# Kernel tuning notes

Hardware: AMD Instinct MI355X
Metric: run time of the kernel (lower is better)

The kernel has to match this reference:

```python
import jax, jax.numpy as jnp
import numpy as np
from jax import lax

D_IN = 512      # input_size
H = 256         # hidden_size
GRU_IN = H + D_IN  # flowdelta_step prepends residual (H) to the input


def setup_inputs() -> dict:
    key = jax.random.key(0)
    kx, k1, k2, k3, k4 = jax.random.split(key, 5)
    B, T = 128, 1024
    x = jax.random.normal(kx, (B, T, D_IN), dtype=jnp.float32)
    # PyTorch GRU parameter layout: weight_ih (3H, in), weight_hh (3H, H),
    # gate order [r, z, n], init U(-1/sqrt(H), 1/sqrt(H))
    s = 1.0 / np.sqrt(H)
    w_ih = jax.random.uniform(k1, (3 * H, GRU_IN), jnp.float32, -s, s)
    w_hh = jax.random.uniform(k2, (3 * H, H), jnp.float32, -s, s)
    b_ih = jax.random.uniform(k3, (3 * H,), jnp.float32, -s, s)
    b_hh = jax.random.uniform(k4, (3 * H,), jnp.float32, -s, s)
    return {"x": x, "w_ih": w_ih, "w_hh": w_hh, "b_ih": b_ih, "b_hh": b_hh}


def reference(x, w_ih, w_hh, b_ih, b_hh):
    # x: (B, T, D). FlowRNN transposes to (T, B, D) and loops over T,
    # feeding one step at a time with carried hidden -> equivalent to a
    # single unidirectional GRU scan whose step input is [residual, x_t],
    # residual_t = h_{t-1} - h_{t-2} (zeros before t=1), logged pre-update.
    B = x.shape[0]
    xs = jnp.swapaxes(x, 0, 1)  # (T, B, D)

    def step(carry, x_t):
        h_prev, res = carry                                  # (B,H), (B,H)
        inp = jnp.concatenate([res, x_t], axis=-1)           # (B, H+D)
        gx = inp @ w_ih.T + b_ih                             # (B, 3H)
        gh = h_prev @ w_hh.T + b_hh                          # (B, 3H)
        r = jax.nn.sigmoid(gx[:, :H] + gh[:, :H])
        z = jax.nn.sigmoid(gx[:, H:2 * H] + gh[:, H:2 * H])
        n = jnp.tanh(gx[:, 2 * H:] + r * gh[:, 2 * H:])
        h_new = (1.0 - z) * n + z * h_prev
        new_res = h_new - h_prev                             # flowdelta
        return (h_new, new_res), (h_new, res)

    h0 = jnp.zeros((B, H), x.dtype)
    res0 = jnp.zeros((B, H), x.dtype)
    _, (outs, ress) = lax.scan(step, (h0, res0), xs)
    output = jnp.swapaxes(outs, 0, 1)           # (B, T, H)
    residual_output = jnp.swapaxes(ress, 0, 1)  # (B, T, H)
    return output, residual_output
```

## Files before the change

kernel.cpp:

```cpp
#include <hip/hip_runtime.h>


typedef __attribute__((ext_vector_type(8))) short bf16x8_t;
typedef __attribute__((ext_vector_type(4))) float f32x4_t;

#define MFMA16(a, b, c) __builtin_amdgcn_mfma_f32_16x16x32_bf16((a), (b), (c), 0, 0, 0)

constexpr int Bb = 128, Tt = 1024, Dd = 512, Hh = 256;
constexpr int Gg = 8;
constexpr int Ss = 8;
constexpr int ROWS = Bb / Gg;
constexpr int Wj = Hh / Ss;

__device__ __forceinline__ short f2bf(float f) {
  union { float f; unsigned int u; } v; v.f = f;
  unsigned int r = v.u + 0x7fffu + ((v.u >> 16) & 1u);
  return (short)(r >> 16);
}

__device__ __forceinline__ bf16x8_t load8_bf(const float* p) {
  const f32x4_t a = *(const f32x4_t*)p;
  const f32x4_t b = *(const f32x4_t*)(p + 4);
  bf16x8_t r;
  r[0] = f2bf(a[0]); r[1] = f2bf(a[1]); r[2] = f2bf(a[2]); r[3] = f2bf(a[3]);
  r[4] = f2bf(b[0]); r[5] = f2bf(b[1]); r[6] = f2bf(b[2]); r[7] = f2bf(b[3]);
  return r;
}

__global__ __launch_bounds__(256, 1)
void flowrnn_scan(const float* __restrict__ x, const float* __restrict__ w_ih,
                  const float* __restrict__ w_hh, const float* __restrict__ b_ih,
                  const float* __restrict__ b_hh, float* __restrict__ out,
                  unsigned int* __restrict__ ws) {
  __shared__ short xstage[ROWS][520];
  __shared__ float accS[ROWS][260];
  __shared__ float hpown[ROWS][Wj];
  __shared__ float biasR[Wj], biasZ[Wj], biasNX[Wj], biasNH[Wj];

  const int tid  = threadIdx.x;
  const int wid  = tid >> 6;
  const int lane = tid & 63;
  const int n16  = lane & 15;
  const int q    = lane >> 4;
  const int g    = blockIdx.x >> 3;
  const int s    = blockIdx.x & 7;
  const int j0   = Wj * s;

  unsigned int* arrive = ws;
  unsigned short* hring = (unsigned short*)(ws + Gg * Tt);
  unsigned short* rring = hring + 2 * Bb * Hh;

  if (tid < Wj) {
    int j = tid;
    biasR[j]  = b_ih[j0 + j]        + b_hh[j0 + j];
    biasZ[j]  = b_ih[256 + j0 + j]  + b_hh[256 + j0 + j];
    biasNX[j] = b_ih[512 + j0 + j];
    biasNH[j] = b_hh[512 + j0 + j];
  }
  ((float*)hpown)[tid] = 0.f;
  ((float*)hpown)[tid + 256] = 0.f;

  bf16x8_t brz[16], bn[8], bxp[16], bxs[8];
  {
    int grow = (wid < 2) ? (j0 + wid * 16 + n16) : (256 + j0 + (wid - 2) * 16 + n16);
    for (int c = 0; c < 8; ++c)
      brz[c] = load8_bf(w_ih + (size_t)grow * 768 + c * 32 + q * 8);
    for (int c = 0; c < 8; ++c)
      brz[8 + c] = load8_bf(w_hh + (size_t)grow * 256 + c * 32 + q * 8);
  }
  if (wid < 2) {
    int grow = 512 + j0 + wid * 16 + n16;
    for (int c = 0; c < 8; ++c)
      bn[c] = load8_bf(w_ih + (size_t)grow * 768 + c * 32 + q * 8);
  } else {
    int grow = 512 + j0 + (wid - 2) * 16 + n16;
    for (int c = 0; c < 8; ++c)
      bn[c] = load8_bf(w_hh + (size_t)grow * 256 + c * 32 + q * 8);
  }
  {
    int tp = (wid == 3) ? 5 : wid * 2;
    int grow = (tp >> 1) * 256 + j0 + (tp & 1) * 16 + n16;
    for (int c = 0; c < 16; ++c)
      bxp[c] = load8_bf(w_ih + (size_t)grow * 768 + 256 + c * 32 + q * 8);
    int ts = (wid < 2) ? 1 : 3;
    int gs = (ts >> 1) * 256 + j0 + (ts & 1) * 16 + n16;
    int cbase = (wid & 1) ? 8 : 0;
    for (int c = 0; c < 8; ++c)
      bxs[c] = load8_bf(w_ih + (size_t)gs * 768 + 256 + (cbase + c) * 32 + q * 8);
  }
  __syncthreads();

  long spin_budget = 30000000;

  for (int t = 0; t < Tt; ++t) {
    {
      int row = tid >> 4, seg = tid & 15;
      const float* xp = x + ((size_t)(g * ROWS + row) * Tt + t) * Dd + seg * 32;
      bf16x8_t v0 = load8_bf(xp);
      bf16x8_t v1 = load8_bf(xp + 8);
      bf16x8_t v2 = load8_bf(xp + 16);
      bf16x8_t v3 = load8_bf(xp + 24);
      bf16x8_t* dst = (bf16x8_t*)&xstage[row][seg * 32];
      dst[0] = v0; dst[1] = v1; dst[2] = v2; dst[3] = v3;
    }
    __syncthreads();

    f32x4_t accP = {0.f, 0.f, 0.f, 0.f}, accSx = {0.f, 0.f, 0.f, 0.f};
    {
      bf16x8_t xa[16];
      for (int c = 0; c < 16; ++c)
        xa[c] = *(const bf16x8_t*)&xstage[n16][c * 32 + q * 8];
      for (int c = 0; c < 16; ++c)
        accP = MFMA16(xa[c], bxp[c], accP);
      int cbase = (wid & 1) ? 8 : 0;
      for (int c = 0; c < 8; ++c)
        accSx = MFMA16(xa[cbase + c], bxs[c], accSx);
    }

    f32x4_t accRZ = {0.f, 0.f, 0.f, 0.f}, accN = {0.f, 0.f, 0.f, 0.f};
    if (t > 0) {
      if (tid == 0) {
        unsigned int* fp = arrive + g * Tt + (t - 1);
        while (__hip_atomic_load(fp, __ATOMIC_RELAXED, __HIP_MEMORY_SCOPE_AGENT) < (unsigned)Ss) {
          __builtin_amdgcn_s_sleep(1);
          if (--spin_budget < 0) break;
        }
        __threadfence();
      }
      __syncthreads();
      const int slot = (t - 1) & 1;
      const unsigned short* hb = hring + (size_t)slot * (Bb * Hh);
      const unsigned short* rb = rring + (size_t)slot * (Bb * Hh);
      const int b = g * ROWS + n16;
      bf16x8_t rf[8], hf[8];
      for (int c = 0; c < 8; ++c) {
        rf[c] = *(const bf16x8_t*)(rb + (size_t)b * Hh + c * 32 + q * 8);
        hf[c] = *(const bf16x8_t*)(hb + (size_t)b * Hh + c * 32 + q * 8);
      }
      for (int c = 0; c < 8; ++c) accRZ = MFMA16(rf[c], brz[c], accRZ);
      for (int c = 0; c < 8; ++c) accRZ = MFMA16(hf[c], brz[8 + c], accRZ);
      if (wid < 2) { for (int c = 0; c < 8; ++c) accN = MFMA16(rf[c], bn[c], accN); }
      else         { for (int c = 0; c < 8; ++c) accN = MFMA16(hf[c], bn[c], accN); }
    }

    {
      const int r0 = q * 4;
      for (int i = 0; i < 4; ++i) accS[r0 + i][wid * 16 + n16] = accRZ[i];
      const int nb = (wid < 2) ? (64 + wid * 16) : (96 + (wid - 2) * 16);
      for (int i = 0; i < 4; ++i) accS[r0 + i][nb + n16] = accN[i];
      const int pc = (wid == 0) ? 128 : (wid == 1) ? 176 : (wid == 2) ? 224 : 240;
      for (int i = 0; i < 4; ++i) accS[r0 + i][pc + n16] = accP[i];
      const int sc = 144 + 16 * wid + ((wid >= 2) ? 16 : 0);
      for (int i = 0; i < 4; ++i) accS[r0 + i][sc + n16] = accSx[i];
    }
    __syncthreads();

    {
      const int row = tid >> 4;
      const int jp = (tid & 15) * 2;
      float hnew[2], resv[2];
      for (int u = 0; u < 2; ++u) {
        const int j = jp + u;
        float ar  = accS[row][j];
        float az  = accS[row][32 + j];
        float anx = accS[row][64 + j];
        float anh = accS[row][96 + j];
        float xr = (j < 16) ? accS[row][128 + j] : (accS[row][144 + j - 16] + accS[row][160 + j - 16]);
        float xz = (j < 16) ? accS[row][176 + j] : (accS[row][192 + j - 16] + accS[row][208 + j - 16]);
        float xn = (j < 16) ? accS[row][224 + j] : accS[row][240 + j - 16];
        float rg = 1.f / (1.f + __expf(-(ar + xr + biasR[j])));
        float zg = 1.f / (1.f + __expf(-(az + xz + biasZ[j])));
        float narg = (anx + xn + biasNX[j]) + rg * (anh + biasNH[j]);
        float e2 = __expf(2.f * narg);
        float ng = 1.f - 2.f / (e2 + 1.f);
        float hp = hpown[row][j];
        float h  = (1.f - zg) * ng + zg * hp;
        hnew[u] = h; resv[u] = h - hp;
        hpown[row][j] = h;
      }
      const int b = g * ROWS + row;
      float* op = out + ((size_t)b * Tt + t) * Hh + j0 + jp;
      op[0] = hnew[0]; op[1] = hnew[1];
      const int slot = t & 1;
      unsigned int hp32 = ((unsigned int)(unsigned short)f2bf(hnew[0])) |
                          ((unsigned int)(unsigned short)f2bf(hnew[1]) << 16);
      unsigned int rp32 = ((unsigned int)(unsigned short)f2bf(resv[0])) |
                          ((unsigned int)(unsigned short)f2bf(resv[1]) << 16);
      unsigned int* hd = (unsigned int*)(hring + (size_t)slot * (Bb * Hh) + (size_t)b * Hh + j0 + jp);
      unsigned int* rd = (unsigned int*)(rring + (size_t)slot * (Bb * Hh) + (size_t)b * Hh + j0 + jp);
      __hip_atomic_store(hd, hp32, __ATOMIC_RELAXED, __HIP_MEMORY_SCOPE_AGENT);
      __hip_atomic_store(rd, rp32, __ATOMIC_RELAXED, __HIP_MEMORY_SCOPE_AGENT);
    }
    __syncthreads();
    if (tid == 0) {
      __threadfence();
      __hip_atomic_fetch_add(arrive + g * Tt + t, 1u, __ATOMIC_RELEASE, __HIP_MEMORY_SCOPE_AGENT);
    }
  }
}

__global__ void flowrnn_resid(const float* __restrict__ out, float* __restrict__ res) {
  size_t i = (size_t)blockIdx.x * blockDim.x + threadIdx.x;
  const size_t total = (size_t)Bb * Tt * (Hh / 4);
  if (i >= total) return;
  const int j4 = (int)(i & 63);
  const int t  = (int)((i >> 6) & 1023);
  const size_t b = i >> 16;
  const f32x4_t* o = (const f32x4_t*)out;
  const size_t base = b * (size_t)Tt * 64 + j4;
  f32x4_t v = {0.f, 0.f, 0.f, 0.f};
  if (t == 1) v = o[base];
  else if (t >= 2) {
    f32x4_t a = o[base + (size_t)(t - 1) * 64];
    f32x4_t c = o[base + (size_t)(t - 2) * 64];
    v = a - c;
  }
  ((f32x4_t*)res)[base + (size_t)t * 64] = v;
}

extern "C" void kernel_launch(void* const* d_in, const int* in_sizes, int n_in,
                              void* d_out, int out_size, void* d_ws, size_t ws_size,
                              hipStream_t stream) {
  const float* x    = (const float*)d_in[0];
  const float* w_ih = (const float*)d_in[1];
  const float* w_hh = (const float*)d_in[2];
  const float* b_ih = (const float*)d_in[3];
  const float* b_hh = (const float*)d_in[4];
  float* out = (float*)d_out;
  float* res = out + (size_t)Bb * Tt * Hh;

  hipMemsetAsync(d_ws, 0, (size_t)Gg * Tt * sizeof(unsigned int), stream);

  flowrnn_scan<<<Gg * Ss, 256, 0, stream>>>(x, w_ih, w_hh, b_ih, b_hh, out,
                                            (unsigned int*)d_ws);

  const size_t total4 = (size_t)Bb * Tt * (Hh / 4);
  flowrnn_resid<<<(int)((total4 + 255) / 256), 256, 0, stream>>>(out, res);
}
```

Baseline: 11.03 ms.

## Use per-wave flag sync, prefetch next x step, and fuse residual output

Each of the 4 waves now increments the arrival counter itself and polls it with a wave-broadcast load, replacing the tid-0 spin plus block barriers and thread fences. The target count becomes Ss*4. The next timestep's x slice is prefetched into registers during the current step, hiding its global-load latency. The residual output is written directly from the scan, so the separate residual kernel and its extra read of the output are removed. Dropping the release fences in favour of relaxed atomics plus s_waitcnt risks memory-ordering bugs, and the larger spin budget only changes the timeout.

After: 10.35 ms. 6.1% less time.

```diff
diff --git a/kernel.cpp b/kernel.cpp
--- a/kernel.cpp
+++ b/kernel.cpp
@@ -11,6 +11,7 @@
 constexpr int Ss = 8;
 constexpr int ROWS = Bb / Gg;
 constexpr int Wj = Hh / Ss;
+constexpr unsigned FLAG_TARGET = Ss * 4;
 
 __device__ __forceinline__ short f2bf(float f) {
   union { float f; unsigned int u; } v; v.f = f;
@@ -25,6 +26,15 @@
   r[0] = f2bf(a[0]); r[1] = f2bf(a[1]); r[2] = f2bf(a[2]); r[3] = f2bf(a[3]);
   r[4] = f2bf(b[0]); r[5] = f2bf(b[1]); r[6] = f2bf(b[2]); r[7] = f2bf(b[3]);
   return r;
+}
+
+__device__ __forceinline__ bf16x8_t ringload(const unsigned short* p) {
+  unsigned long long lo = __hip_atomic_load((const unsigned long long*)p,
+                                            __ATOMIC_RELAXED, __HIP_MEMORY_SCOPE_AGENT);
+  unsigned long long hi = __hip_atomic_load((const unsigned long long*)(p + 4),
+                                            __ATOMIC_RELAXED, __HIP_MEMORY_SCOPE_AGENT);
+  union { unsigned long long u[2]; bf16x8_t v; } r;
+  r.u[0] = lo; r.u[1] = hi; return r.v;
 }
 
 __global__ __launch_bounds__(256, 1)
@@ -49,6 +59,7 @@
   unsigned int* arrive = ws;
   unsigned short* hring = (unsigned short*)(ws + Gg * Tt);
   unsigned short* rring = hring + 2 * Bb * Hh;
+  float* rout = out + (size_t)Bb * Tt * Hh;
 
   if (tid < Wj) {
     int j = tid;
@@ -88,22 +99,38 @@
     for (int c = 0; c < 8; ++c)
       bxs[c] = load8_bf(w_ih + (size_t)gs * 768 + 256 + (cbase + c) * 32 + q * 8);
   }
+
+  const int xrow = tid >> 4, xseg = tid & 15;
+  const float* xbase = x + (size_t)(g * ROWS + xrow) * Tt * Dd + xseg * 32;
+  f32x4_t xpre[8];
+  {
+    const f32x4_t* xp = (const f32x4_t*)(xbase);
+#pragma unroll
+    for (int i = 0; i < 8; ++i) xpre[i] = xp[i];
+  }
   __syncthreads();
 
-  long spin_budget = 30000000;
+  long spin_budget = 50000000;
 
   for (int t = 0; t < Tt; ++t) {
     {
-      int row = tid >> 4, seg = tid & 15;
-      const float* xp = x + ((size_t)(g * ROWS + row) * Tt + t) * Dd + seg * 32;
-      bf16x8_t v0 = load8_bf(xp);
-      bf16x8_t v1 = load8_bf(xp + 8);
-      bf16x8_t v2 = load8_bf(xp + 16);
-      bf16x8_t v3 = load8_bf(xp + 24);
-      bf16x8_t* dst = (bf16x8_t*)&xstage[row][seg * 32];
-      dst[0] = v0; dst[1] = v1; dst[2] = v2; dst[3] = v3;
+      bf16x8_t* dst = (bf16x8_t*)&xstage[xrow][xseg * 32];
+#pragma unroll
+      for (int i = 0; i < 4; ++i) {
+        f32x4_t a = xpre[2 * i], b = xpre[2 * i + 1];
+        bf16x8_t v;
+        v[0] = f2bf(a[0]); v[1] = f2bf(a[1]); v[2] = f2bf(a[2]); v[3] = f2bf(a[3]);
+        v[4] = f2bf(b[0]); v[5] = f2bf(b[1]); v[6] = f2bf(b[2]); v[7] = f2bf(b[3]);
+        dst[i] = v;
+      }
     }
     __syncthreads();
+
+    if (t + 1 < Tt) {
+      const f32x4_t* xp = (const f32x4_t*)(xbase + (size_t)(t + 1) * Dd);
+#pragma unroll
+      for (int i = 0; i < 8; ++i) xpre[i] = xp[i];
+    }
 
     f32x4_t accP = {0.f, 0.f, 0.f, 0.f}, accSx = {0.f, 0.f, 0.f, 0.f};
     {
@@ -119,23 +146,24 @@
 
     f32x4_t accRZ = {0.f, 0.f, 0.f, 0.f}, accN = {0.f, 0.f, 0.f, 0.f};
     if (t > 0) {
-      if (tid == 0) {
-        unsigned int* fp = arrive + g * Tt + (t - 1);
-        while (__hip_atomic_load(fp, __ATOMIC_RELAXED, __HIP_MEMORY_SCOPE_AGENT) < (unsigned)Ss) {
-          __builtin_amdgcn_s_sleep(1);
-          if (--spin_budget < 0) break;
-        }
-        __threadfence();
-      }
-      __syncthreads();
+      const unsigned int* fp = arrive + g * Tt + (t - 1);
+      for (;;) {
+        unsigned int v = 0;
+        if (lane == 0)
+          v = __hip_atomic_load(fp, __ATOMIC_RELAXED, __HIP_MEMORY_SCOPE_AGENT);
+        v = (unsigned int)__shfl((int)v, 0, 64);
+        if (v >= FLAG_TARGET) break;
+        __builtin_amdgcn_s_sleep(1);
+        if (--spin_budget < 0) break;
+      }
       const int slot = (t - 1) & 1;
       const unsigned short* hb = hring + (size_t)slot * (Bb * Hh);
       const unsigned short* rb = rring + (size_t)slot * (Bb * Hh);
       const int b = g * ROWS + n16;
       bf16x8_t rf[8], hf[8];
       for (int c = 0; c < 8; ++c) {
-        rf[c] = *(const bf16x8_t*)(rb + (size_t)b * Hh + c * 32 + q * 8);
-        hf[c] = *(const bf16x8_t*)(hb + (size_t)b * Hh + c * 32 + q * 8);
+        rf[c] = ringload(rb + (size_t)b * Hh + c * 32 + q * 8);
+        hf[c] = ringload(hb + (size_t)b * Hh + c * 32 + q * 8);
       }
       for (int c = 0; c < 8; ++c) accRZ = MFMA16(rf[c], brz[c], accRZ);
       for (int c = 0; c < 8; ++c) accRZ = MFMA16(hf[c], brz[8 + c], accRZ);
@@ -157,8 +185,9 @@
 
     {
       const int row = tid >> 4;
-      const int jp = (tid & 15) * 2;
+      const int jp  = (tid & 15) * 2;
       float hnew[2], resv[2];
+#pragma unroll
       for (int u = 0; u < 2; ++u) {
         const int j = jp + u;
         float ar  = accS[row][j];
@@ -176,11 +205,8 @@
         float hp = hpown[row][j];
         float h  = (1.f - zg) * ng + zg * hp;
         hnew[u] = h; resv[u] = h - hp;
-        hpown[row][j] = h;
       }
       const int b = g * ROWS + row;
-      float* op = out + ((size_t)b * Tt + t) * Hh + j0 + jp;
-      op[0] = hnew[0]; op[1] = hnew[1];
       const int slot = t & 1;
       unsigned int hp32 = ((unsigned int)(unsigned short)f2bf(hnew[0])) |
                           ((unsigned int)(unsigned short)f2bf(hnew[1]) << 16);
@@ -190,32 +216,25 @@
       unsigned int* rd = (unsigned int*)(rring + (size_t)slot * (Bb * Hh) + (size_t)b * Hh + j0 + jp);
       __hip_atomic_store(hd, hp32, __ATOMIC_RELAXED, __HIP_MEMORY_SCOPE_AGENT);
       __hip_atomic_store(rd, rp32, __ATOMIC_RELAXED, __HIP_MEMORY_SCOPE_AGENT);
-    }
-    __syncthreads();
-    if (tid == 0) {
-      __threadfence();
-      __hip_atomic_fetch_add(arrive + g * Tt + t, 1u, __ATOMIC_RELEASE, __HIP_MEMORY_SCOPE_AGENT);
-    }
-  }
-}
-
-__global__ void flowrnn_resid(const float* __restrict__ out, float* __restrict__ res) {
-  size_t i = (size_t)blockIdx.x * blockDim.x + threadIdx.x;
-  const size_t total = (size_t)Bb * Tt * (Hh / 4);
-  if (i >= total) return;
-  const int j4 = (int)(i & 63);
-  const int t  = (int)((i >> 6) & 1023);
-  const size_t b = i >> 16;
-  const f32x4_t* o = (const f32x4_t*)out;
-  const size_t base = b * (size_t)Tt * 64 + j4;
-  f32x4_t v = {0.f, 0.f, 0.f, 0.f};
-  if (t == 1) v = o[base];
-  else if (t >= 2) {
-    f32x4_t a = o[base + (size_t)(t - 1) * 64];
-    f32x4_t c = o[base + (size_t)(t - 2) * 64];
-    v = a - c;
-  }
-  ((f32x4_t*)res)[base + (size_t)t * 64] = v;
+      float* op = out + ((size_t)b * Tt + t) * Hh + j0 + jp;
+      op[0] = hnew[0]; op[1] = hnew[1];
+      if (t == 0) {
+        float* rp0 = rout + ((size_t)b * Tt) * Hh + j0 + jp;
+        rp0[0] = 0.f; rp0[1] = 0.f;
+      }
+      if (t + 1 < Tt) {
+        float* rp = rout + ((size_t)b * Tt + t + 1) * Hh + j0 + jp;
+        rp[0] = resv[0]; rp[1] = resv[1];
+      }
+      hpown[row][jp]     = hnew[0];
+      hpown[row][jp + 1] = hnew[1];
+    }
+
+    __builtin_amdgcn_s_waitcnt(0);
+    if (lane == 0)
+      __hip_atomic_fetch_add(arrive + g * Tt + t, 1u,
+                             __ATOMIC_RELAXED, __HIP_MEMORY_SCOPE_AGENT);
+  }
 }
 
 extern "C" void kernel_launch(void* const* d_in, const int* in_sizes, int n_in,
@@ -227,13 +246,9 @@
   const float* b_ih = (const float*)d_in[3];
   const float* b_hh = (const float*)d_in[4];
   float* out = (float*)d_out;
-  float* res = out + (size_t)Bb * Tt * Hh;
 
   hipMemsetAsync(d_ws, 0, (size_t)Gg * Tt * sizeof(unsigned int), stream);
 
   flowrnn_scan<<<Gg * Ss, 256, 0, stream>>>(x, w_ih, w_hh, b_ih, b_hh, out,
                                             (unsigned int*)d_ws);
-
-  const size_t total4 = (size_t)Bb * Tt * (Hh / 4);
-  flowrnn_resid<<<(int)((total4 + 255) / 256), 256, 0, stream>>>(out, res);
-}
+}
```
